# Optimization experiments

Hardware: AMD Instinct MI355X
Metric: run time of the kernel (lower is better)

## Reference

```python
import jax, jax.numpy as jnp
import numpy as np
import math

N_HEADS = 8
N_LAYERS = 2
HYPER1 = 0.6
HYPER2 = 0.07


def setup_inputs() -> dict:
    key = jax.random.key(0)
    ks = jax.random.split(key, 32)
    B, S, D, M = 32, 512, 768, 384  # M = mem_dim = D // 2
    rn = lambda k, shape, scale: jax.random.normal(k, shape, jnp.float32) * scale
    sd, sm = 1.0 / math.sqrt(D), 1.0 / math.sqrt(M)
    inp = {
        'gcn_inputs': rn(ks[0], (B, S, D), 1.0),
        'adj_matrix': jax.random.uniform(ks[1], (B, S, S), jnp.float32),
        'attn_mask': jax.random.randint(ks[2], (B, 1, S), 0, 2).astype(jnp.int32),
        's_mask': jax.random.randint(ks[3], (B, S), 0, 2).astype(jnp.int32),
        'a_mask': jax.random.randint(ks[4], (B, S), 0, 2).astype(jnp.int32),
        # MultiHeadAttention: two Linear(d_model, d_model) for q and k
        'Wq': rn(ks[5], (D, D), sd), 'bq': jnp.zeros((D,), jnp.float32),
        'Wk': rn(ks[6], (D, D), sd), 'bk': jnp.zeros((D,), jnp.float32),
        # semW / depW: layer0 D->M, layer1 M->M
        'semW0': rn(ks[7], (D, M), sd), 'semb0': jnp.zeros((M,), jnp.float32),
        'semW1': rn(ks[8], (M, M), sm), 'semb1': jnp.zeros((M,), jnp.float32),
        'depW0': rn(ks[9], (D, M), sd), 'depb0': jnp.zeros((M,), jnp.float32),
        'depW1': rn(ks[10], (M, M), sm), 'depb1': jnp.zeros((M,), jnp.float32),
        # projection head fc1: M->32, fc2: 32->M
        'fc1W': rn(ks[11], (M, 32), sm), 'fc1b': jnp.zeros((32,), jnp.float32),
        'fc2W': rn(ks[12], (32, M), 1.0 / math.sqrt(32)), 'fc2b': jnp.zeros((M,), jnp.float32),
        # fc3: M->M, fc4: D->M
        'fc3W': rn(ks[13], (M, M), sm), 'fc3b': jnp.zeros((M,), jnp.float32),
        'fc4W': rn(ks[14], (D, M), sd), 'fc4b': jnp.zeros((M,), jnp.float32),
    }
    return inp


def _sim(z1, z2):
    # F.normalize(dim=2) then bmm
    n1 = z1 / jnp.maximum(jnp.linalg.norm(z1, axis=2, keepdims=True), 1e-12)
    n2 = z2 / jnp.maximum(jnp.linalg.norm(z2, axis=2, keepdims=True), 1e-12)
    return jnp.einsum('bsd,btd->bst', n1, n2)


def _diag(m):
    return jnp.diagonal(m, axis1=-2, axis2=-1)


def _scope_semi_loss(z1, z2, sm, am):
    f = lambda x: jnp.exp(x / HYPER2)
    a_z1 = z1 * am[..., None]
    m_between = f(_sim(a_z1, z2))
    m_refl = f(_sim(a_z1, z1))
    s_z1 = z1 * sm[..., None]
    s_z2 = z2 * sm[..., None]
    as_refl = f(_sim(a_z1, s_z1))
    as_between = f(_sim(a_z1, s_z2))
    w = _sim(a_z1, s_z2)
    weighted = f(w * _diag(w)[..., None])
    pos = (_diag(as_between)
           + (as_refl.sum(2) - _diag(as_refl))
           + (weighted.sum(2) - _diag(weighted)))
    alle = m_refl.sum(2) + m_between.sum(2) - _diag(m_refl)
    return -jnp.log(pos / alle)


def reference(gcn_inputs, adj_matrix, attn_mask, s_mask, a_mask,
              Wq, bq, Wk, bk,
              semW0, semb0, semW1, semb1,
              depW0, depb0, depW1, depb1,
              fc1W, fc1b, fc2W, fc2b, fc3W, fc3b, fc4W, fc4b):
    B, S, D = gcn_inputs.shape
    h, dk = N_HEADS, D // N_HEADS

    # ---- MultiHeadAttention -> per-head attention adjacency ----
    q = (gcn_inputs @ Wq + bq).reshape(B, S, h, dk).transpose(0, 2, 1, 3)
    k = (gcn_inputs @ Wk + bk).reshape(B, S, h, dk).transpose(0, 2, 1, 3)
    scores = jnp.einsum('bhsd,bhtd->bhst', q, k) / math.sqrt(dk)
    scores = jnp.where(attn_mask[:, None] == 0, -10000.0, scores)  # [B,1,1,S] broadcast
    attn = jax.nn.softmax(scores, axis=-1)  # dropout in eval mode -> identity

    # average heads, zero diagonal, add identity, row-mask by encoder atts
    adj_ag = attn.mean(axis=1)  # [B,S,S]
    eye = jnp.eye(S, dtype=adj_ag.dtype)
    adj_ag = adj_ag * (1.0 - eye) + eye
    atts = attn_mask.astype(adj_ag.dtype)  # text_encoder_atts [B,1,S]
    adj_ag = jnp.swapaxes(atts, 1, 2) * adj_ag

    # ---- gated dual-GCN layers ----
    sem_params = [(semW0, semb0), (semW1, semb1)]
    dep_params = [(depW0, depb0), (depW1, depb1)]
    H_l = gcn_inputs
    I_sem = None
    for l in range(N_LAYERS):
        sW, sb = sem_params[l]
        dW, db = dep_params[l]
        AH_sem = jnp.einsum('bst,btd->bsd', adj_ag, H_l)
        I_sem = AH_sem @ sW + sb
        AH_dep = jnp.einsum('bst,btd->bsd', adj_matrix, H_l)
        I_dep = AH_dep @ dW + db
        g = jax.nn.sigmoid(I_dep)
        I_dep_g = HYPER1 * g
        I_com = (1.0 - I_dep_g) * I_sem + I_dep_g * I_dep
        H_out = jax.nn.relu(I_com @ fc3W + fc3b)
        if l == 0:
            H_l = H_l @ fc4W + fc4b
        g_l = jax.nn.sigmoid(H_l)
        H_l = g_l * H_out + (1.0 - g_l) * H_l

    # ---- projection + symmetric contrastive scope loss ----
    proj = lambda z: jax.nn.elu(z @ fc1W + fc1b) @ fc2W + fc2b
    h1 = proj(H_l)
    h2 = proj(I_sem)
    smf = s_mask.astype(h1.dtype)
    amf = a_mask.astype(h1.dtype)
    l1 = _scope_semi_loss(h1, h2, smf, amf)
    l2 = _scope_semi_loss(h2, h1, smf, amf)
    loss = (l1 + l2) * 0.5
    loss_cl = loss.mean(axis=1, keepdims=True).mean()
    return loss_cl
```

## Files before the change

### kernel.cpp

```cpp
#include <hip/hip_runtime.h>
#include <math.h>


typedef __bf16 bf16x8 __attribute__((ext_vector_type(8)));
typedef __bf16 bf16x4 __attribute__((ext_vector_type(4)));
typedef float f32x4 __attribute__((ext_vector_type(4)));

__device__ __forceinline__ void glds16(const void* g, void* l) {
    __builtin_amdgcn_global_load_lds(
        (const __attribute__((address_space(1))) unsigned*)g,
        (__attribute__((address_space(3))) unsigned*)l, 16, 0, 0);
}

__device__ __forceinline__ float sigf(float x) { return 1.f / (1.f + __expf(-x)); }

__global__ __launch_bounds__(256) void mfma_gemm(
    const __bf16* __restrict__ A, const __bf16* __restrict__ B,
    const float* __restrict__ bias, int bzDiv, int bzStride,
    const __bf16* __restrict__ E,
    float* __restrict__ Cf, __bf16* __restrict__ Cb,
    int K, int lda, int ldb, int ldc, int nMax,
    long sAo, long sAi, long sBo, long sBi, int zInner, long sC, int act)
{
    __shared__ __bf16 As[3][128 * 32];
    __shared__ __bf16 Bs[3][128 * 32];
    int z = blockIdx.z;

    int gx = gridDim.x, gy = gridDim.y;
    int lin = blockIdx.x + gx * blockIdx.y;
    const int GRP = 8;
    int per = GRP * gy;
    int grp = lin / per, rr = lin - grp * per;
    int x0 = grp * GRP;
    int width = (gx - x0 < GRP) ? (gx - x0) : GRP;
    int bx = x0 + rr % width, by = rr / width;

    long aBase = (long)(z / zInner) * sAo + (long)(z % zInner) * sAi;
    long bBase = (long)(z / zInner) * sBo + (long)(z % zInner) * sBi;
    long cBase = (long)z * sC;
    int m0 = bx * 128, n0 = by * 128;
    int tid = threadIdx.x;
    int wave = tid >> 6, lane = tid & 63;
    int wm = wave >> 1, wn = wave & 1;

    int e0 = tid, e1 = tid + 256;
    int r0 = e0 >> 2, r1 = e1 >> 2;
    int q0 = (e0 & 3) ^ (r0 & 3) ^ ((r0 >> 2) & 3);
    int q1 = (e1 & 3) ^ (r1 & 3) ^ ((r1 >> 2) & 3);
    const __bf16* Ag0 = A + aBase + (long)(m0 + r0) * lda + q0 * 8;
    const __bf16* Ag1 = A + aBase + (long)(m0 + r1) * lda + q1 * 8;
    const __bf16* Bg0 = B + bBase + (long)(n0 + r0) * ldb + q0 * 8;
    const __bf16* Bg1 = B + bBase + (long)(n0 + r1) * ldb + q1 * 8;

    f32x4 acc[4][4];
#pragma unroll
    for (int i = 0; i < 4; i++)
#pragma unroll
        for (int j = 0; j < 4; j++) acc[i][j] = (f32x4){0.f, 0.f, 0.f, 0.f};

    int rl = lane & 15;
    int quad = lane >> 4;
    int qs = quad ^ (rl & 3) ^ ((rl >> 2) & 3);
    int arow = wm * 64 + rl;
    int brow = wn * 64 + rl;

    int nk = K >> 5;
    glds16(Ag0, As[0] + e0 * 8); glds16(Ag1, As[0] + e1 * 8);
    glds16(Bg0, Bs[0] + e0 * 8); glds16(Bg1, Bs[0] + e1 * 8);
    if (nk > 1) {
        glds16(Ag0 + 32, As[1] + e0 * 8); glds16(Ag1 + 32, As[1] + e1 * 8);
        glds16(Bg0 + 32, Bs[1] + e0 * 8); glds16(Bg1 + 32, Bs[1] + e1 * 8);
    }

    int bi = 0;
    for (int i = 0; i < nk; ++i) {
        __builtin_amdgcn_sched_barrier(0);
        if (i + 1 < nk) asm volatile("s_waitcnt vmcnt(4) lgkmcnt(0)" ::: "memory");
        else            asm volatile("s_waitcnt vmcnt(0) lgkmcnt(0)" ::: "memory");
        __builtin_amdgcn_s_barrier();
        if (i + 2 < nk) {
            int pb = bi + 2; if (pb >= 3) pb -= 3;
            int ko = (i + 2) * 32;
            glds16(Ag0 + ko, As[pb] + e0 * 8); glds16(Ag1 + ko, As[pb] + e1 * 8);
            glds16(Bg0 + ko, Bs[pb] + e0 * 8); glds16(Bg1 + ko, Bs[pb] + e1 * 8);
        }
        const bf16x8* Asv = (const bf16x8*)As[bi];
        const bf16x8* Bsv = (const bf16x8*)Bs[bi];
        bf16x8 af[4], bfr[4];
#pragma unroll
        for (int mi = 0; mi < 4; mi++) af[mi] = Asv[(arow + mi * 16) * 4 + qs];
#pragma unroll
        for (int ni = 0; ni < 4; ni++) bfr[ni] = Bsv[(brow + ni * 16) * 4 + qs];
#pragma unroll
        for (int mi = 0; mi < 4; mi++)
#pragma unroll
            for (int ni = 0; ni < 4; ni++)
                acc[mi][ni] = __builtin_amdgcn_mfma_f32_16x16x32_bf16(
                    af[mi], bfr[ni], acc[mi][ni], 0, 0, 0);
        bi++; if (bi >= 3) bi -= 3;
    }

    int crow = m0 + wm * 64 + (lane >> 4) * 4;
    int ccol = n0 + wn * 64 + (lane & 15);
    const float* biasz = bias ? bias + (z / bzDiv) * bzStride : nullptr;
    float bv[4];
#pragma unroll
    for (int ni = 0; ni < 4; ni++) {
        int col = ccol + ni * 16;
        bv[ni] = (biasz && col < nMax) ? biasz[col] : 0.f;
    }
#pragma unroll
    for (int mi = 0; mi < 4; mi++) {
#pragma unroll
        for (int ni = 0; ni < 4; ni++) {
            int col = ccol + ni * 16;
            if (col >= nMax) continue;
#pragma unroll
            for (int r = 0; r < 4; r++) {
                float v = acc[mi][ni][r] + bv[ni];
                long idx = cBase + (long)(crow + mi * 16 + r) * ldc + col;
                if (act == 1) v = fmaxf(v, 0.f);
                else if (act == 2) v = (v > 0.f) ? v : expm1f(v);
                else if (act == 4) {
                    float e = (float)E[idx];
                    v = fmaxf(v, 0.f);
                    float g = sigf(e);
                    v = g * v + (1.f - g) * e;
                }
                if (Cf) Cf[idx] = v;
                if (Cb) Cb[idx] = (__bf16)v;
            }
        }
    }
}

struct WCast {
    const float* src[10];
    unsigned dstOff[10];
    int R[10], C[10];
    int start[11];
};

__global__ __launch_bounds__(256) void castW_kernel(WCast wc, __bf16* wb)
{
    __shared__ float t[32][33];
    int bid = blockIdx.x;
    int e = 0;
    while (bid >= wc.start[e + 1]) e++;
    int tt = bid - wc.start[e];
    int cT = wc.C[e] >> 5;
    int ty = tt / cT, tx = tt - ty * cT;
    const float* in = wc.src[e];
    __bf16* out = wb + wc.dstOff[e];
    int R = wc.R[e], C = wc.C[e];
    int r0 = ty * 32, c0 = tx * 32;
    int tid = threadIdx.x;
    int r = tid >> 3, c4 = (tid & 7) * 4;
    float4 v = *(const float4*)(in + (long)(r0 + r) * C + c0 + c4);
    t[r][c4] = v.x; t[r][c4 + 1] = v.y; t[r][c4 + 2] = v.z; t[r][c4 + 3] = v.w;
    __syncthreads();
    int c = tid >> 3, r4 = (tid & 7) * 4;
    bf16x4 o;
    o[0] = (__bf16)t[r4 + 0][c]; o[1] = (__bf16)t[r4 + 1][c];
    o[2] = (__bf16)t[r4 + 2][c]; o[3] = (__bf16)t[r4 + 3][c];
    *(bf16x4*)(out + (long)(c0 + c) * R + r0 + r4) = o;
}

__global__ void cast_bf16_kernel(const float* __restrict__ in, __bf16* __restrict__ out, long n4)
{
    long i = (long)blockIdx.x * blockDim.x + threadIdx.x;
    if (i < n4) {
        float4 v = ((const float4*)in)[i];
        bf16x4 o; o[0] = (__bf16)v.x; o[1] = (__bf16)v.y; o[2] = (__bf16)v.z; o[3] = (__bf16)v.w;
        ((bf16x4*)out)[i] = o;
    }
}

__global__ __launch_bounds__(256) void softmax_combine(
    const __bf16* __restrict__ scores, const int* __restrict__ attn_mask,
    __bf16* __restrict__ adj_agb, int b0)
{
    const int S = 512;
    int s = blockIdx.x, bl = blockIdx.y, b = b0 + bl;
    int tid = threadIdx.x;
    const float scale = 0.1020620726159658f;
    int t0 = tid, t1 = tid + 256;
    int cm0 = attn_mask[b * S + t0], cm1 = attn_mask[b * S + t1];
    float vals[8][2], part[8];
#pragma unroll
    for (int h = 0; h < 8; ++h) {
        long rb = ((long)(bl * 8 + h) * S + s) * S;
        float r0 = (float)scores[rb + t0], r1 = (float)scores[rb + t1];
        vals[h][0] = cm0 ? __expf(r0 * scale) : 0.f;
        vals[h][1] = cm1 ? __expf(r1 * scale) : 0.f;
        part[h] = vals[h][0] + vals[h][1];
    }
    __shared__ float red[4][8];
    __shared__ float linv[8];
    int lane = tid & 63, w = tid >> 6;
#pragma unroll
    for (int h = 0; h < 8; ++h) {
        float v = part[h];
        for (int o = 32; o > 0; o >>= 1) v += __shfl_down(v, o);
        if (lane == 0) red[w][h] = v;
    }
    __syncthreads();
    if (tid < 8) {
        float l = red[0][tid] + red[1][tid] + red[2][tid] + red[3][tid];
        linv[tid] = 1.f / fmaxf(l, 1e-30f);
    }
    __syncthreads();
    float rowmask = attn_mask[b * S + s] ? 1.f : 0.f;
    float a0 = 0.f, a1 = 0.f;
#pragma unroll
    for (int h = 0; h < 8; ++h) { a0 += vals[h][0] * linv[h]; a1 += vals[h][1] * linv[h]; }
    a0 *= 0.125f; a1 *= 0.125f;
    if (t0 == s) a0 = 1.f;
    if (t1 == s) a1 = 1.f;
    long ob = ((long)b * S + s) * S;
    adj_agb[ob + t0] = (__bf16)(rowmask * a0);
    adj_agb[ob + t1] = (__bf16)(rowmask * a1);
}

__global__ void gcn_combine2(const __bf16* __restrict__ IsIdb,
                             __bf16* __restrict__ Icomb, long n8)
{
    long i = (long)blockIdx.x * blockDim.x + threadIdx.x;
    if (i >= n8) return;
    bf16x8 sv = ((const bf16x8*)IsIdb)[i];
    bf16x8 dv = ((const bf16x8*)(IsIdb + n8 * 8))[i];
    bf16x8 o;
#pragma unroll
    for (int j = 0; j < 8; j++) {
        float s = (float)sv[j], d = (float)dv[j];
        float g = 0.6f * sigf(d);
        o[j] = (__bf16)((1.f - g) * s + g * d);
    }
    ((bf16x8*)Icomb)[i] = o;
}

__global__ __launch_bounds__(128) void rownorm(__bf16* __restrict__ hb, int Dm)
{
    __bf16* p = hb + (long)blockIdx.x * Dm;
    int tid = threadIdx.x;
    float ss = 0.f;
    for (int i = tid; i < Dm; i += 128) { float v = (float)p[i]; ss += v * v; }
    for (int o = 32; o > 0; o >>= 1) ss += __shfl_down(ss, o);
    __shared__ float sb[2];
    __shared__ float scale;
    if ((tid & 63) == 0) sb[tid >> 6] = ss;
    __syncthreads();
    if (tid == 0) scale = 1.f / fmaxf(sqrtf(sb[0] + sb[1]), 1e-12f);
    __syncthreads();
    for (int i = tid; i < Dm; i += 128) p[i] = (__bf16)((float)p[i] * scale);
}

__global__ __launch_bounds__(256) void loss_kernel(
    const __bf16* __restrict__ G11, const __bf16* __restrict__ G12,
    const __bf16* __restrict__ G22,
    const int* __restrict__ s_mask, const int* __restrict__ a_mask,
    float* __restrict__ lossb)
{
    const int S = 512;
    int s = blockIdx.x, b = blockIdx.y;
    int tid = threadIdx.x;
    if (a_mask[b * S + s] == 0) {
        if (tid == 0) lossb[b * S + s] = 0.f;
        return;
    }
    long base = ((long)b * S + s) * S;
    long cbase = (long)b * S * S + s;
    const float it = 1.f / 0.07f;
    float sms = s_mask[b * S + s] ? 1.f : 0.f;
    float d12 = (float)G12[base + s];
    float w1i = sms * d12 * it, w2i = w1i;
    float p[8];
#pragma unroll
    for (int h = 0; h < 8; h++) p[h] = 0.f;
#pragma unroll
    for (int j = 0; j < 2; j++) {
        int t = tid + j * 256;
        bool smt = s_mask[b * S + t] != 0;
        bool off = (t != s);
        float g11 = (float)G11[base + t], g12 = (float)G12[base + t];
        float g21 = (float)G12[cbase + (long)t * S];
        float g22 = (float)G22[base + t];
        float e11 = __expf(g11 * it), e12 = __expf(g12 * it);
        float e21 = __expf(g21 * it), e22 = __expf(g22 * it);
        p[2] += e11; p[3] += e12; p[6] += e22; p[7] += e21;
        if (off) {
            p[0] += smt ? e11 : 1.f;
            p[4] += smt ? e22 : 1.f;
            p[1] += smt ? __expf(g12 * w1i) : 1.f;
            p[5] += smt ? __expf(g21 * w2i) : 1.f;
        }
    }
    __shared__ float red[4][8];
    int lane = tid & 63, w = tid >> 6;
#pragma unroll
    for (int h = 0; h < 8; h++) {
        float v = p[h];
        for (int o = 32; o > 0; o >>= 1) v += __shfl_down(v, o);
        if (lane == 0) red[w][h] = v;
    }
    __syncthreads();
    if (tid == 0) {
        float r[8];
#pragma unroll
        for (int h = 0; h < 8; h++) r[h] = red[0][h] + red[1][h] + red[2][h] + red[3][h];
        float g11ss = (float)G11[base + s], g22ss = (float)G22[base + s];
        float pos1 = __expf(w1i) + r[0] + r[1];
        float alle1 = r[2] - __expf(g11ss * it) + r[3];
        float pos2 = __expf(w2i) + r[4] + r[5];
        float alle2 = r[6] - __expf(g22ss * it) + r[7];
        lossb[b * S + s] = 0.5f * ((__logf(alle1) - __logf(pos1)) +
                                   (__logf(alle2) - __logf(pos2)));
    }
}

__global__ __launch_bounds__(256) void final_reduce(
    const float* __restrict__ lossb, float* __restrict__ out, int n)
{
    int tid = threadIdx.x;
    float s = 0.f;
    for (int i = tid; i < n; i += 256) s += lossb[i];
    for (int o = 32; o > 0; o >>= 1) s += __shfl_down(s, o);
    __shared__ float sb[4];
    if ((tid & 63) == 0) sb[tid >> 6] = s;
    __syncthreads();
    if (tid == 0) out[0] = (sb[0] + sb[1] + sb[2] + sb[3]) / (float)n;
}

static inline void mg(hipStream_t st, const __bf16* A, const __bf16* B,
                      const float* bias, int bzDiv, int bzStride,
                      const __bf16* E, float* Cf, __bf16* Cb,
                      int M, int Npad, int nMax, int K, int lda, int ldb, int ldc,
                      long sAo, long sAi, long sBo, long sBi, int zInner, long sC, int nz,
                      int act)
{
    dim3 g(M / 128, Npad / 128, nz);
    mfma_gemm<<<g, 256, 0, st>>>(A, B, bias, bzDiv, bzStride, E, Cf, Cb,
                                 K, lda, ldb, ldc, nMax,
                                 sAo, sAi, sBo, sBi, zInner, sC, act);
}

extern "C" void kernel_launch(void* const* d_in, const int* in_sizes, int n_in,
                              void* d_out, int out_size, void* d_ws, size_t ws_size,
                              hipStream_t stream)
{
    const int B = 32, S = 512, D = 768, Mm = 384;
    const int MT = B * S;
    const float* X    = (const float*)d_in[0];
    const float* adjm = (const float*)d_in[1];
    const int* attn_mask = (const int*)d_in[2];
    const int* s_mask    = (const int*)d_in[3];
    const int* a_mask    = (const int*)d_in[4];
    const float* Wq = (const float*)d_in[5],  *bq = (const float*)d_in[6];
    const float* Wk = (const float*)d_in[7],  *bk = (const float*)d_in[8];
    const float* semW0 = (const float*)d_in[9],  *semb0 = (const float*)d_in[10];
    const float* semW1 = (const float*)d_in[11], *semb1 = (const float*)d_in[12];
    const float* depW0 = (const float*)d_in[13], *depb0 = (const float*)d_in[14];
    const float* depW1 = (const float*)d_in[15], *depb1 = (const float*)d_in[16];
    const float* fc1W = (const float*)d_in[17], *fc1b = (const float*)d_in[18];
    const float* fc2W = (const float*)d_in[19], *fc2b = (const float*)d_in[20];
    const float* fc3W = (const float*)d_in[21], *fc3b = (const float*)d_in[22];
    const float* fc4W = (const float*)d_in[23], *fc4b = (const float*)d_in[24];

    char* ws = (char*)d_ws;
    const size_t MB = 1u << 20;
    const size_t KB = 1u << 10;

    __bf16* Xb      = (__bf16*)(ws + 0 * MB);
    __bf16* adj_agb = (__bf16*)(ws + 24 * MB);
    __bf16* adjmb   = (__bf16*)(ws + 40 * MB);
    __bf16* qkb     = (__bf16*)(ws + 56 * MB);
    __bf16* scoreB  = (__bf16*)(ws + 104 * MB);
    __bf16* P64     = (__bf16*)(ws + 56 * MB);
    __bf16* IsIdb   = (__bf16*)(ws + 80 * MB);
    __bf16* Isemb   = IsIdb;
    __bf16* Icomb   = (__bf16*)(ws + 104 * MB);
    __bf16* Hpreb   = (__bf16*)(ws + 116 * MB);
    __bf16* Hb      = (__bf16*)(ws + 128 * MB);
    __bf16* t1b     = (__bf16*)(ws + 0 * MB);
    __bf16* hb12    = (__bf16*)(ws + 140 * MB);
    __bf16* h1b     = hb12;
    __bf16* h2b     = hb12 + (long)MT * Mm;
    __bf16* G11     = (__bf16*)(ws + 24 * MB);
    __bf16* G12     = (__bf16*)(ws + 40 * MB);
    __bf16* G22     = (__bf16*)(ws + 72 * MB);

    char* wreg = ws + 192 * MB;
    __bf16* wb     = (__bf16*)wreg;
    __bf16* WqkT   = (__bf16*)(wreg + 0 * KB);
    __bf16* semW0T = (__bf16*)(wreg + 2304 * KB);
    __bf16* depW0T = (__bf16*)(wreg + 2880 * KB);
    __bf16* fc4WT  = (__bf16*)(wreg + 3456 * KB);
    __bf16* semW1T = (__bf16*)(wreg + 4032 * KB);
    __bf16* depW1T = (__bf16*)(wreg + 4320 * KB);
    __bf16* fc3WT  = (__bf16*)(wreg + 4608 * KB);
    __bf16* fc1WT  = (__bf16*)(wreg + 4896 * KB);
    __bf16* fc2WT  = (__bf16*)(wreg + 4992 * KB);
    float*  bqk    = (float*)(wreg + 5016 * KB);
    float*  sbd0   = (float*)(wreg + 5024 * KB);
    float*  sbd1   = (float*)(wreg + 5028 * KB);
    float*  lossb  = (float*)(wreg + 5036 * KB);

    long nSM = (long)S * Mm, nSS = (long)S * S;
    long nPM = (long)Mm * S;

    cast_bf16_kernel<<<(MT * D / 4 + 255) / 256, 256, 0, stream>>>(X, Xb, (long)MT * D / 4);
    cast_bf16_kernel<<<((long)B * nSS / 4 + 255) / 256, 256, 0, stream>>>(adjm, adjmb, (long)B * nSS / 4);
    {
        WCast wc;
        const float* srcs[10] = {Wq, Wk, semW0, depW0, fc4W, semW1, depW1, fc3W, fc1W, fc2W};
        unsigned offs[10] = {0u, 589824u, 1179648u, 1474560u, 1769472u,
                             2064384u, 2211840u, 2359296u, 2506752u, 2555904u};
        int Rs[10] = {768, 768, 768, 768, 768, 384, 384, 384, 384, 32};
        int Cs[10] = {768, 768, 384, 384, 384, 384, 384, 384, 32, 384};
        int st = 0;
        for (int i = 0; i < 10; i++) {
            wc.src[i] = srcs[i]; wc.dstOff[i] = offs[i];
            wc.R[i] = Rs[i]; wc.C[i] = Cs[i];
            wc.start[i] = st; st += (Rs[i] / 32) * (Cs[i] / 32);
        }
        wc.start[10] = st;
        castW_kernel<<<st, 256, 0, stream>>>(wc, wb);
    }
    hipMemsetAsync(fc1WT + 32 * Mm, 0, (size_t)96 * Mm * 2, stream);
    hipMemcpyAsync(bqk, bq, D * 4, hipMemcpyDeviceToDevice, stream);
    hipMemcpyAsync(bqk + D, bk, D * 4, hipMemcpyDeviceToDevice, stream);
    hipMemcpyAsync(sbd0, semb0, Mm * 4, hipMemcpyDeviceToDevice, stream);
    hipMemcpyAsync(sbd0 + Mm, depb0, Mm * 4, hipMemcpyDeviceToDevice, stream);
    hipMemcpyAsync(sbd1, semb1, Mm * 4, hipMemcpyDeviceToDevice, stream);
    hipMemcpyAsync(sbd1 + Mm, depb1, Mm * 4, hipMemcpyDeviceToDevice, stream);

    mg(stream, Xb, WqkT, bqk, 1, 0, nullptr, nullptr, qkb, MT, 1536, 1536, D,
       D, D, 1536, 0, 0, 0, 0, 1, 0, 1, 0);

    for (int c = 0; c < 2; c++) {
        const __bf16* qc = qkb + (long)c * 16 * S * 1536;
        mg(stream, qc, qc + 768, nullptr, 1, 0, nullptr, nullptr, scoreB, S, S, S, 96,
           1536, 1536, S, (long)S * 1536, 96, (long)S * 1536, 96, 8, nSS, 128, 0);
        softmax_combine<<<dim3(S, 16), 256, 0, stream>>>(scoreB, attn_mask, adj_agb, c * 16);
    }

    long n8 = (long)MT * Mm / 8;
    int cwg = (int)((n8 + 255) / 256);

    mg(stream, semW0T, Xb, nullptr, 1, 0, nullptr, nullptr, P64, Mm, S, S, D,
       D, D, S, (long)Mm * D, 0, 0, (long)S * D, 32, nPM, 64, 0);
    mg(stream, adj_agb, P64, sbd0, 32, Mm, nullptr, nullptr, IsIdb, S, Mm, Mm, S,
       S, S, Mm, 0, nSS, 0, nPM, 64, nSM, 64, 0);
    gcn_combine2<<<cwg, 256, 0, stream>>>(IsIdb, Icomb, n8);
    mg(stream, Xb, fc4WT, fc4b, 1, 0, nullptr, nullptr, Hpreb, MT, Mm, Mm, D,
       D, D, Mm, 0, 0, 0, 0, 1, 0, 1, 0);
    mg(stream, Icomb, fc3WT, fc3b, 1, 0, Hpreb, nullptr, Hb, MT, Mm, Mm, Mm,
       Mm, Mm, Mm, 0, 0, 0, 0, 1, 0, 1, 4);

    mg(stream, semW1T, Hb, nullptr, 1, 0, nullptr, nullptr, P64, Mm, S, S, Mm,
       Mm, Mm, S, (long)Mm * Mm, 0, 0, nSM, 32, nPM, 64, 0);
    mg(stream, adj_agb, P64, sbd1, 32, Mm, nullptr, nullptr, IsIdb, S, Mm, Mm, S,
       S, S, Mm, 0, nSS, 0, nPM, 64, nSM, 64, 0);
    gcn_combine2<<<cwg, 256, 0, stream>>>(IsIdb, Icomb, n8);
    mg(stream, Icomb, fc3WT, fc3b, 1, 0, Hb, nullptr, Hb, MT, Mm, Mm, Mm,
       Mm, Mm, Mm, 0, 0, 0, 0, 1, 0, 1, 4);

    long sAproj = (long)(Isemb - Hb);
    mg(stream, Hb, fc1WT, fc1b, 1, 0, nullptr, nullptr, t1b, MT, 128, 32, Mm,
       Mm, Mm, 32, 0, sAproj, 0, 0, 2, (long)MT * 32, 2, 2);
    mg(stream, t1b, fc2WT, fc2b, 1, 0, nullptr, nullptr, hb12, MT, Mm, Mm, 32,
       32, 32, Mm, 0, (long)MT * 32, 0, 0, 2, (long)MT * Mm, 2, 0);

    rownorm<<<2 * MT, 128, 0, stream>>>(hb12, Mm);

    mg(stream, h1b, h1b, nullptr, 1, 0, nullptr, nullptr, G11, S, S, S, Mm,
       Mm, Mm, S, 0, nSM, 32 * nSM, nSM, 32, nSS, 64, 0);
    mg(stream, h2b, h2b, nullptr, 1, 0, nullptr, nullptr, G22, S, S, S, Mm,
       Mm, Mm, S, 0, nSM, 0, nSM, 32, nSS, 32, 0);

    loss_kernel<<<dim3(S, B), 256, 0, stream>>>(G11, G12, G22, s_mask, a_mask, lossb);
    final_reduce<<<1, 256, 0, stream>>>(lossb, (float*)d_out, MT);
}
```

Measured before the change: 803.6 us.

## Widen GEMM tile to 128x256 with double-buffered LDS and per-wave column strips

Measured after the change: 1.248 ms. 55.3% more time.

```diff
diff --git a/kernel.cpp b/kernel.cpp
--- a/kernel.cpp
+++ b/kernel.cpp
@@ -22,8 +22,8 @@
     int K, int lda, int ldb, int ldc, int nMax,
     long sAo, long sAi, long sBo, long sBi, int zInner, long sC, int act)
 {
-    __shared__ __bf16 As[3][128 * 32];
-    __shared__ __bf16 Bs[3][128 * 32];
+    __shared__ __bf16 As[2][128 * 32];
+    __shared__ __bf16 Bs[2][256 * 32];
     int z = blockIdx.z;
 
     int gx = gridDim.x, gy = gridDim.y;
@@ -38,70 +38,67 @@
     long aBase = (long)(z / zInner) * sAo + (long)(z % zInner) * sAi;
     long bBase = (long)(z / zInner) * sBo + (long)(z % zInner) * sBi;
     long cBase = (long)z * sC;
-    int m0 = bx * 128, n0 = by * 128;
+    int m0 = bx * 128, n0 = by * 256;
     int tid = threadIdx.x;
     int wave = tid >> 6, lane = tid & 63;
-    int wm = wave >> 1, wn = wave & 1;
-
-    int e0 = tid, e1 = tid + 256;
-    int r0 = e0 >> 2, r1 = e1 >> 2;
-    int q0 = (e0 & 3) ^ (r0 & 3) ^ ((r0 >> 2) & 3);
-    int q1 = (e1 & 3) ^ (r1 & 3) ^ ((r1 >> 2) & 3);
-    const __bf16* Ag0 = A + aBase + (long)(m0 + r0) * lda + q0 * 8;
-    const __bf16* Ag1 = A + aBase + (long)(m0 + r1) * lda + q1 * 8;
-    const __bf16* Bg0 = B + bBase + (long)(n0 + r0) * ldb + q0 * 8;
-    const __bf16* Bg1 = B + bBase + (long)(n0 + r1) * ldb + q1 * 8;
-
-    f32x4 acc[4][4];
-#pragma unroll
-    for (int i = 0; i < 4; i++)
+    int rl = lane & 15, quad = lane >> 4;
+    int qs = quad ^ (rl & 3) ^ ((rl >> 2) & 3);
+
+    const __bf16* Ag[2];
+    const __bf16* Bg[4];
+#pragma unroll
+    for (int j = 0; j < 2; j++) {
+        int c = tid + j * 256, r = c >> 2;
+        int q = (c & 3) ^ (r & 3) ^ ((r >> 2) & 3);
+        Ag[j] = A + aBase + (long)(m0 + r) * lda + q * 8;
+    }
+#pragma unroll
+    for (int j = 0; j < 4; j++) {
+        int c = tid + j * 256, r = c >> 2;
+        int q = (c & 3) ^ (r & 3) ^ ((r >> 2) & 3);
+        Bg[j] = B + bBase + (long)(n0 + r) * ldb + q * 8;
+    }
+
+    f32x4 acc[8][4];
+#pragma unroll
+    for (int i = 0; i < 8; i++)
 #pragma unroll
         for (int j = 0; j < 4; j++) acc[i][j] = (f32x4){0.f, 0.f, 0.f, 0.f};
 
-    int rl = lane & 15;
-    int quad = lane >> 4;
-    int qs = quad ^ (rl & 3) ^ ((rl >> 2) & 3);
-    int arow = wm * 64 + rl;
-    int brow = wn * 64 + rl;
-
     int nk = K >> 5;
-    glds16(Ag0, As[0] + e0 * 8); glds16(Ag1, As[0] + e1 * 8);
-    glds16(Bg0, Bs[0] + e0 * 8); glds16(Bg1, Bs[0] + e1 * 8);
-    if (nk > 1) {
-        glds16(Ag0 + 32, As[1] + e0 * 8); glds16(Ag1 + 32, As[1] + e1 * 8);
-        glds16(Bg0 + 32, Bs[1] + e0 * 8); glds16(Bg1 + 32, Bs[1] + e1 * 8);
-    }
-
-    int bi = 0;
+    glds16(Ag[0], As[0] + tid * 8);
+    glds16(Ag[1], As[0] + (tid + 256) * 8);
+#pragma unroll
+    for (int j = 0; j < 4; j++)
+        glds16(Bg[j], Bs[0] + (tid + j * 256) * 8);
+
     for (int i = 0; i < nk; ++i) {
-        __builtin_amdgcn_sched_barrier(0);
-        if (i + 1 < nk) asm volatile("s_waitcnt vmcnt(4) lgkmcnt(0)" ::: "memory");
-        else            asm volatile("s_waitcnt vmcnt(0) lgkmcnt(0)" ::: "memory");
-        __builtin_amdgcn_s_barrier();
-        if (i + 2 < nk) {
-            int pb = bi + 2; if (pb >= 3) pb -= 3;
-            int ko = (i + 2) * 32;
-            glds16(Ag0 + ko, As[pb] + e0 * 8); glds16(Ag1 + ko, As[pb] + e1 * 8);
-            glds16(Bg0 + ko, Bs[pb] + e0 * 8); glds16(Bg1 + ko, Bs[pb] + e1 * 8);
+        __syncthreads();
+        if (i + 1 < nk) {
+            int nb = (i + 1) & 1, ko = (i + 1) * 32;
+            glds16(Ag[0] + ko, As[nb] + tid * 8);
+            glds16(Ag[1] + ko, As[nb] + (tid + 256) * 8);
+#pragma unroll
+            for (int j = 0; j < 4; j++)
+                glds16(Bg[j] + ko, Bs[nb] + (tid + j * 256) * 8);
         }
-        const bf16x8* Asv = (const bf16x8*)As[bi];
-        const bf16x8* Bsv = (const bf16x8*)Bs[bi];
-        bf16x8 af[4], bfr[4];
-#pragma unroll
-        for (int mi = 0; mi < 4; mi++) af[mi] = Asv[(arow + mi * 16) * 4 + qs];
-#pragma unroll
-        for (int ni = 0; ni < 4; ni++) bfr[ni] = Bsv[(brow + ni * 16) * 4 + qs];
-#pragma unroll
-        for (int mi = 0; mi < 4; mi++)
+        const bf16x8* Asv = (const bf16x8*)As[i & 1];
+        const bf16x8* Bsv = (const bf16x8*)Bs[i & 1];
+        bf16x8 af[8], bfr[4];
+#pragma unroll
+        for (int mi = 0; mi < 8; mi++) af[mi] = Asv[(mi * 16 + rl) * 4 + qs];
+#pragma unroll
+        for (int ni = 0; ni < 4; ni++) bfr[ni] = Bsv[(wave * 64 + ni * 16 + rl) * 4 + qs];
+#pragma unroll
+        for (int mi = 0; mi < 8; mi++)
 #pragma unroll
             for (int ni = 0; ni < 4; ni++)
                 acc[mi][ni] = __builtin_amdgcn_mfma_f32_16x16x32_bf16(
                     af[mi], bfr[ni], acc[mi][ni], 0, 0, 0);
-        bi++; if (bi >= 3) bi -= 3;
-    }
-
-    int crow = m0 + wm * 64 + (lane >> 4) * 4;
-    int ccol = n0 + wn * 64 + (lane & 15);
+    }
+
+    int crow = m0 + (lane >> 4) * 4;
+    int ccol = n0 + wave * 64 + (lane & 15);
     const float* biasz = bias ? bias + (z / bzDiv) * bzStride : nullptr;
     float bv[4];
 #pragma unroll
@@ -110,7 +107,7 @@
         bv[ni] = (biasz && col < nMax) ? biasz[col] : 0.f;
     }
 #pragma unroll
-    for (int mi = 0; mi < 4; mi++) {
+    for (int mi = 0; mi < 8; mi++) {
 #pragma unroll
         for (int ni = 0; ni < 4; ni++) {
             int col = ccol + ni * 16;
@@ -338,7 +335,7 @@
                       long sAo, long sAi, long sBo, long sBi, int zInner, long sC, int nz,
                       int act)
 {
-    dim3 g(M / 128, Npad / 128, nz);
+    dim3 g(M / 128, Npad / 256, nz);
     mfma_gemm<<<g, 256, 0, st>>>(A, B, bias, bzDiv, bzStride, E, Cf, Cb,
                                  K, lda, ldb, ldc, nMax,
                                  sAo, sAi, sBo, sBi, zInner, sC, act);
@@ -439,7 +436,7 @@
 
     for (int c = 0; c < 2; c++) {
         const __bf16* qc = qkb + (long)c * 16 * S * 1536;
-        mg(stream, qc, qc + 768, nullptr, 1, 0, nullptr, nullptr, scoreB, S, S, S, 96,
+        mg(stream, qc, qc + 768, nullptr, 1, 0, nullptr, nullptr, scoreB, S, 512, S, 96,
            1536, 1536, S, (long)S * 1536, 96, (long)S * 1536, 96, 8, nSS, 128, 0);
         softmax_combine<<<dim3(S, 16), 256, 0, stream>>>(scoreB, attn_mask, adj_agb, c * 16);
     }
@@ -447,35 +444,35 @@
     long n8 = (long)MT * Mm / 8;
     int cwg = (int)((n8 + 255) / 256);
 
-    mg(stream, semW0T, Xb, nullptr, 1, 0, nullptr, nullptr, P64, Mm, S, S, D,
+    mg(stream, semW0T, Xb, nullptr, 1, 0, nullptr, nullptr, P64, Mm, 512, S, D,
        D, D, S, (long)Mm * D, 0, 0, (long)S * D, 32, nPM, 64, 0);
-    mg(stream, adj_agb, P64, sbd0, 32, Mm, nullptr, nullptr, IsIdb, S, Mm, Mm, S,
+    mg(stream, adj_agb, P64, sbd0, 32, Mm, nullptr, nullptr, IsIdb, S, 512, Mm, S,
        S, S, Mm, 0, nSS, 0, nPM, 64, nSM, 64, 0);
     gcn_combine2<<<cwg, 256, 0, stream>>>(IsIdb, Icomb, n8);
-    mg(stream, Xb, fc4WT, fc4b, 1, 0, nullptr, nullptr, Hpreb, MT, Mm, Mm, D,
+    mg(stream, Xb, fc4WT, fc4b, 1, 0, nullptr, nullptr, Hpreb, MT, 512, Mm, D,
        D, D, Mm, 0, 0, 0, 0, 1, 0, 1, 0);
-    mg(stream, Icomb, fc3WT, fc3b, 1, 0, Hpreb, nullptr, Hb, MT, Mm, Mm, Mm,
+    mg(stream, Icomb, fc3WT, fc3b, 1, 0, Hpreb, nullptr, Hb, MT, 512, Mm, Mm,
        Mm, Mm, Mm, 0, 0, 0, 0, 1, 0, 1, 4);
 
-    mg(stream, semW1T, Hb, nullptr, 1, 0, nullptr, nullptr, P64, Mm, S, S, Mm,
+    mg(stream, semW1T, Hb, nullptr, 1, 0, nullptr, nullptr, P64, Mm, 512, S, Mm,
        Mm, Mm, S, (long)Mm * Mm, 0, 0, nSM, 32, nPM, 64, 0);
-    mg(stream, adj_agb, P64, sbd1, 32, Mm, nullptr, nullptr, IsIdb, S, Mm, Mm, S,
+    mg(stream, adj_agb, P64, sbd1, 32, Mm, nullptr, nullptr, IsIdb, S, 512, Mm, S,
        S, S, Mm, 0, nSS, 0, nPM, 64, nSM, 64, 0);
     gcn_combine2<<<cwg, 256, 0, stream>>>(IsIdb, Icomb, n8);
-    mg(stream, Icomb, fc3WT, fc3b, 1, 0, Hb, nullptr, Hb, MT, Mm, Mm, Mm,
+    mg(stream, Icomb, fc3WT, fc3b, 1, 0, Hb, nullptr, Hb, MT, 512, Mm, Mm,
        Mm, Mm, Mm, 0, 0, 0, 0, 1, 0, 1, 4);
 
     long sAproj = (long)(Isemb - Hb);
-    mg(stream, Hb, fc1WT, fc1b, 1, 0, nullptr, nullptr, t1b, MT, 128, 32, Mm,
+    mg(stream, Hb, fc1WT, fc1b, 1, 0, nullptr, nullptr, t1b, MT, 256, 32, Mm,
        Mm, Mm, 32, 0, sAproj, 0, 0, 2, (long)MT * 32, 2, 2);
-    mg(stream, t1b, fc2WT, fc2b, 1, 0, nullptr, nullptr, hb12, MT, Mm, Mm, 32,
+    mg(stream, t1b, fc2WT, fc2b, 1, 0, nullptr, nullptr, hb12, MT, 512, Mm, 32,
        32, 32, Mm, 0, (long)MT * 32, 0, 0, 2, (long)MT * Mm, 2, 0);
 
     rownorm<<<2 * MT, 128, 0, stream>>>(hb12, Mm);
 
-    mg(stream, h1b, h1b, nullptr, 1, 0, nullptr, nullptr, G11, S, S, S, Mm,
+    mg(stream, h1b, h1b, nullptr, 1, 0, nullptr, nullptr, G11, S, 512, S, Mm,
        Mm, Mm, S, 0, nSM, 32 * nSM, nSM, 32, nSS, 64, 0);
-    mg(stream, h2b, h2b, nullptr, 1, 0, nullptr, nullptr, G22, S, S, S, Mm,
+    mg(stream, h2b, h2b, nullptr, 1, 0, nullptr, nullptr, G22, S, 512, S, Mm,
        Mm, Mm, S, 0, nSM, 0, nSM, 32, nSS, 32, 0);
 
     loss_kernel<<<dim3(S, B), 256, 0, stream>>>(G11, G12, G22, s_mask, a_mask, lossb);
```
